# Kernel tuning notes

Measured on AMD Instinct MI355X. Metric: run time of the kernel, lower is better.

The kernel has to match this reference:

```python
import jax, jax.numpy as jnp
import numpy as np

B, NQ, NKV = 8, 2048, 2048
DQ, DKV, H = 1024, 1024, 256


def setup_inputs() -> dict:
    key = jax.random.key(0)
    ks = jax.random.split(key, 12)
    s = 0.02
    return {
        "x_q": jax.random.normal(ks[0], (B, NQ, DQ), jnp.float32),
        "x_kv": jax.random.normal(ks[1], (B, NKV, DKV), jnp.float32),
        "bias": jax.random.normal(ks[2], (B, NQ, NKV), jnp.float32),
        "wq_w": jax.random.normal(ks[3], (DQ, H), jnp.float32) * s,
        "wq_b": jnp.zeros((H,), jnp.float32),
        "wk_w": jax.random.normal(ks[4], (DKV, H), jnp.float32) * s,
        "wk_b": jnp.zeros((H,), jnp.float32),
        "wv_w": jax.random.normal(ks[5], (DKV, H), jnp.float32) * s,
        "wv_b": jnp.zeros((H,), jnp.float32),
        "f2_w": jax.random.normal(ks[6], (H, H), jnp.float32) * s,
        "f2_b": jnp.zeros((H,), jnp.float32),
    }


def reference(x_q, x_kv, bias, wq_w, wq_b, wk_w, wk_b, wv_w, wv_b, f2_w, f2_b):
    # Projections: [B, nq, H], [B, nkv, H]
    Q = jnp.einsum('bsd,dh->bsh', x_q, wq_w) + wq_b
    K = jnp.einsum('btd,dh->bth', x_kv, wk_w) + wk_b
    V = jnp.einsum('btd,dh->bth', x_kv, wv_w) + wv_b
    exp_w = jnp.exp(bias)          # [B, nq, nkv]
    exp_K = jnp.exp(K)             # [B, nkv, H]
    num = jnp.einsum('bst,bth->bsh', exp_w, exp_K * V)
    den = jnp.einsum('bst,bth->bsh', exp_w, exp_K)
    Yt = jax.nn.sigmoid(Q) * (num / den)
    return jnp.einsum('bsh,hg->bsg', Yt, f2_w) + f2_b
```

## Files before the change

kernel.cpp:

```cpp
#include <hip/hip_runtime.h>
#include <cstddef>
#include <cstdint>

#define BATCH 8
#define NQ    2048
#define NKV   2048
#define DIN   1024
#define HD    256

typedef __attribute__((ext_vector_type(8))) short bf16x8;
typedef __attribute__((ext_vector_type(4))) float f32x4;

__device__ __forceinline__ float sigmoidf_(float x) {
    return 1.0f / (1.0f + expf(-x));
}

__device__ __forceinline__ unsigned short f2bf(float f) {
    union { float f; unsigned int u; } v;
    v.f = f;
    unsigned int u = v.u;
    return (unsigned short)((u + 0x7FFFu + ((u >> 16) & 1u)) >> 16);
}

#define GLL16(gp, lp)                                                        \
    __builtin_amdgcn_global_load_lds(                                        \
        (const __attribute__((address_space(1))) void*)(gp),                 \
        (__attribute__((address_space(3))) void*)(lp), 16, 0, 0)

__device__ __forceinline__ f32x4 gload4(const float* p) {
    f32x4 r;
    asm volatile("global_load_dwordx4 %0, %1, off"
                 : "=v"(r) : "v"(p) : "memory");
    return r;
}

__global__ __launch_bounds__(256)
void wtrans_kernel(const float* __restrict__ w0, const float* __restrict__ w1,
                   const float* __restrict__ w2,
                   unsigned short* __restrict__ t0, unsigned short* __restrict__ t1,
                   unsigned short* __restrict__ t2)
{
    const float* w = (blockIdx.z == 0) ? w0 : (blockIdx.z == 1) ? w1 : w2;
    unsigned short* t = (blockIdx.z == 0) ? t0 : (blockIdx.z == 1) ? t1 : t2;
    const int k0 = blockIdx.y * 64;
    const int n0 = blockIdx.x * 64;
    const int tid = threadIdx.x;
    const int kq = tid >> 4;
    const int nq = tid & 15;
    float4 r[4];
#pragma unroll
    for (int i = 0; i < 4; ++i)
        r[i] = *(const float4*)&w[(size_t)(k0 + kq * 4 + i) * HD + n0 + nq * 4];
#pragma unroll
    for (int j = 0; j < 4; ++j) {
        ushort4 o;
        o.x = f2bf(((const float*)&r[0])[j]);
        o.y = f2bf(((const float*)&r[1])[j]);
        o.z = f2bf(((const float*)&r[2])[j]);
        o.w = f2bf(((const float*)&r[3])[j]);
        *(ushort4*)&t[(size_t)(n0 + nq * 4 + j) * DIN + k0 + kq * 4] = o;
    }
}

#define TS 64
#define TH 256
#define TK 32
#define A_LD 40

__global__ __launch_bounds__(256, 1)
void proj_q_mfma(const float* __restrict__ X,
                 const unsigned short* __restrict__ WT,
                 const float* __restrict__ bv,
                 float* __restrict__ sigQ)
{
    __shared__ unsigned short As[2][TS][A_LD];
    __shared__ unsigned short Bs[2][TH * TK];

    const int m0 = blockIdx.x * TS;
    const int tid = threadIdx.x;
    const int lane = tid & 63, wave = tid >> 6;
    const int quad = lane >> 4, l16 = lane & 15;

    const int a_row = tid >> 2, a_koff = (tid & 3) * 8;
    const float* aP = X + (size_t)(m0 + a_row) * DIN + a_koff;

    const unsigned short* bP[4];
    int ldsOff[4];
#pragma unroll
    for (int j = 0; j < 4; ++j) {
        int idx = j * 256 + tid;
        int row = idx >> 2, c = idx & 3;
        int kc = c ^ ((row >> 1) & 3);
        bP[j] = WT + (size_t)row * DIN + kc * 8;
        ldsOff[j] = (j * 256 + wave * 64) * 16;
    }

    f32x4 acc[4][4] = {};

#pragma unroll
    for (int j = 0; j < 4; ++j)
        GLL16(bP[j], (char*)&Bs[0][0] + ldsOff[j]);
    f32x4 c0 = gload4(aP);
    f32x4 c1 = gload4(aP + 4);
    f32x4 n0 = gload4(aP + TK);
    f32x4 n1 = gload4(aP + TK + 4);

    for (int k0 = 0; k0 < DIN; k0 += TK) {
        const int p = (k0 >> 5) & 1, pn = p ^ 1;
        const int kb = (k0 + TK < DIN) ? (k0 + TK) : (DIN - TK);
        const int km = (k0 + 2 * TK < DIN) ? (k0 + 2 * TK) : (DIN - TK);
        char* bL = (char*)&Bs[pn][0];
#pragma unroll
        for (int j = 0; j < 4; ++j)
            GLL16(bP[j] + kb, bL + ldsOff[j]);
        asm volatile("s_waitcnt vmcnt(4)" : "+v"(c0), "+v"(c1) :: "memory");
        ushort4 q0, q1;
        q0.x = f2bf(c0[0]); q0.y = f2bf(c0[1]); q0.z = f2bf(c0[2]); q0.w = f2bf(c0[3]);
        q1.x = f2bf(c1[0]); q1.y = f2bf(c1[1]); q1.z = f2bf(c1[2]); q1.w = f2bf(c1[3]);
        *(ushort4*)&As[p][a_row][a_koff]     = q0;
        *(ushort4*)&As[p][a_row][a_koff + 4] = q1;
        f32x4 m0v = gload4(aP + km);
        f32x4 m1v = gload4(aP + km + 4);
        asm volatile("s_waitcnt lgkmcnt(0)\ns_barrier" ::: "memory");
        bf16x8 af[4], bf[4];
#pragma unroll
        for (int rt = 0; rt < 4; ++rt)
            af[rt] = *(const bf16x8*)&As[p][rt * 16 + l16][quad * 8];
#pragma unroll
        for (int ct = 0; ct < 4; ++ct) {
            int row = wave * 64 + ct * 16 + l16;
            int off = row * 64 + ((quad ^ ((row >> 1) & 3)) * 16);
            bf[ct] = *(const bf16x8*)((const char*)&Bs[p][0] + off);
        }
#pragma unroll
        for (int rt = 0; rt < 4; ++rt)
#pragma unroll
            for (int ct = 0; ct < 4; ++ct)
                acc[rt][ct] = __builtin_amdgcn_mfma_f32_16x16x32_bf16(
                    af[rt], bf[ct], acc[rt][ct], 0, 0, 0);
        asm volatile("s_barrier" ::: "memory");
        c0 = n0; c1 = n1; n0 = m0v; n1 = m1v;
    }

#pragma unroll
    for (int rt = 0; rt < 4; ++rt)
#pragma unroll
        for (int ct = 0; ct < 4; ++ct) {
            const int h = wave * 64 + ct * 16 + l16;
            const float bb = bv[h];
#pragma unroll
            for (int r = 0; r < 4; ++r) {
                const int m = m0 + rt * 16 + quad * 4 + r;
                sigQ[(size_t)m * HD + h] = sigmoidf_(acc[rt][ct][r] + bb);
            }
        }
}

__global__ __launch_bounds__(256, 1)
void proj_kv_mfma(const float* __restrict__ X,
                  const unsigned short* __restrict__ WKT,
                  const float* __restrict__ bk,
                  const unsigned short* __restrict__ WVT,
                  const float* __restrict__ bvv,
                  unsigned short* __restrict__ eKt,
                  unsigned short* __restrict__ eKVt)
{
    __shared__ unsigned short As[2][TS][A_LD];
    __shared__ unsigned short Bk[2][TH * TK];
    __shared__ unsigned short Bv[2][TH * TK];

    const int m0 = blockIdx.x * TS;
    const int tid = threadIdx.x;
    const int lane = tid & 63, wave = tid >> 6;
    const int quad = lane >> 4, l16 = lane & 15;

    const int a_row = tid >> 2, a_koff = (tid & 3) * 8;
    const float* aP = X + (size_t)(m0 + a_row) * DIN + a_koff;

    const unsigned short* bkP[4];
    const unsigned short* bvP[4];
    int ldsOff[4];
#pragma unroll
    for (int j = 0; j < 4; ++j) {
        int idx = j * 256 + tid;
        int row = idx >> 2, c = idx & 3;
        int kc = c ^ ((row >> 1) & 3);
        bkP[j] = WKT + (size_t)row * DIN + kc * 8;
        bvP[j] = WVT + (size_t)row * DIN + kc * 8;
        ldsOff[j] = (j * 256 + wave * 64) * 16;
    }

    f32x4 acck[4][4] = {};
    f32x4 accv[4][4] = {};

#pragma unroll
    for (int j = 0; j < 4; ++j) {
        GLL16(bkP[j], (char*)&Bk[0][0] + ldsOff[j]);
        GLL16(bvP[j], (char*)&Bv[0][0] + ldsOff[j]);
    }
    f32x4 c0 = gload4(aP);
    f32x4 c1 = gload4(aP + 4);
    f32x4 n0 = gload4(aP + TK);
    f32x4 n1 = gload4(aP + TK + 4);

    for (int k0 = 0; k0 < DIN; k0 += TK) {
        const int p = (k0 >> 5) & 1, pn = p ^ 1;
        const int kb = (k0 + TK < DIN) ? (k0 + TK) : (DIN - TK);
        const int km = (k0 + 2 * TK < DIN) ? (k0 + 2 * TK) : (DIN - TK);
        char* bkL = (char*)&Bk[pn][0];
        char* bvL = (char*)&Bv[pn][0];
#pragma unroll
        for (int j = 0; j < 4; ++j) {
            GLL16(bkP[j] + kb, bkL + ldsOff[j]);
            GLL16(bvP[j] + kb, bvL + ldsOff[j]);
        }
        asm volatile("s_waitcnt vmcnt(8)" : "+v"(c0), "+v"(c1) :: "memory");
        ushort4 q0, q1;
        q0.x = f2bf(c0[0]); q0.y = f2bf(c0[1]); q0.z = f2bf(c0[2]); q0.w = f2bf(c0[3]);
        q1.x = f2bf(c1[0]); q1.y = f2bf(c1[1]); q1.z = f2bf(c1[2]); q1.w = f2bf(c1[3]);
        *(ushort4*)&As[p][a_row][a_koff]     = q0;
        *(ushort4*)&As[p][a_row][a_koff + 4] = q1;
        f32x4 m0v = gload4(aP + km);
        f32x4 m1v = gload4(aP + km + 4);
        asm volatile("s_waitcnt lgkmcnt(0)\ns_barrier" ::: "memory");
        bf16x8 af[4], bkf[4], bvf[4];
#pragma unroll
        for (int rt = 0; rt < 4; ++rt)
            af[rt] = *(const bf16x8*)&As[p][rt * 16 + l16][quad * 8];
#pragma unroll
        for (int ct = 0; ct < 4; ++ct) {
            int row = wave * 64 + ct * 16 + l16;
            int off = row * 64 + ((quad ^ ((row >> 1) & 3)) * 16);
            bkf[ct] = *(const bf16x8*)((const char*)&Bk[p][0] + off);
            bvf[ct] = *(const bf16x8*)((const char*)&Bv[p][0] + off);
        }
#pragma unroll
        for (int rt = 0; rt < 4; ++rt)
#pragma unroll
            for (int ct = 0; ct < 4; ++ct) {
                acck[rt][ct] = __builtin_amdgcn_mfma_f32_16x16x32_bf16(
                    af[rt], bkf[ct], acck[rt][ct], 0, 0, 0);
                accv[rt][ct] = __builtin_amdgcn_mfma_f32_16x16x32_bf16(
                    af[rt], bvf[ct], accv[rt][ct], 0, 0, 0);
            }
        asm volatile("s_barrier" ::: "memory");
        c0 = n0; c1 = n1; n0 = m0v; n1 = m1v;
    }

    const int bidx = m0 >> 11;
    const int tb = m0 & (NKV - 1);
#pragma unroll
    for (int rt = 0; rt < 4; ++rt)
#pragma unroll
        for (int ct = 0; ct < 4; ++ct) {
            const int h = wave * 64 + ct * 16 + l16;
            const float bkb = bk[h];
            const float bvb = bvv[h];
            ushort4 pk, pv;
            unsigned short* pK = (unsigned short*)&pk;
            unsigned short* pV = (unsigned short*)&pv;
#pragma unroll
            for (int r = 0; r < 4; ++r) {
                float e  = __expf(acck[rt][ct][r] + bkb);
                float ev = e * (accv[rt][ct][r] + bvb);
                pK[r] = f2bf(e);
                pV[r] = f2bf(ev);
            }
            const int t0 = tb + rt * 16 + quad * 4;
            size_t base = ((size_t)bidx * HD + h) * NKV + t0;
            *(ushort4*)&eKt[base]  = pk;
            *(ushort4*)&eKVt[base] = pv;
        }
}

__global__ __launch_bounds__(256, 1)
void aft_mfma_kernel(const float* __restrict__ bias,
                     const unsigned short* __restrict__ eKt,
                     const unsigned short* __restrict__ eKVt,
                     const float* __restrict__ sigQ,
                     float* __restrict__ Yt)
{
    __shared__ unsigned short As[2][TS][A_LD];
    __shared__ unsigned short Bn[2][TH * TK];
    __shared__ unsigned short Bd[2][TH * TK];

    const int lin = blockIdx.y * gridDim.x + blockIdx.x;
    const int b   = lin & 7;
    const int s0  = (lin >> 3) * TS;
    const int tid = threadIdx.x;
    const int lane = tid & 63, wave = tid >> 6;
    const int quad = lane >> 4, l16 = lane & 15;

    const int a_row = tid >> 2, a_koff = (tid & 3) * 8;
    const float* aP = bias + ((size_t)b * NQ + (s0 + a_row)) * NKV + a_koff;

    const unsigned short* bnP[4];
    const unsigned short* bdP[4];
    int ldsOff[4];
#pragma unroll
    for (int j = 0; j < 4; ++j) {
        int idx = j * 256 + tid;
        int row = idx >> 2, c = idx & 3;
        int kc = c ^ ((row >> 1) & 3);
        bnP[j] = eKVt + ((size_t)b * HD + row) * NKV + kc * 8;
        bdP[j] = eKt  + ((size_t)b * HD + row) * NKV + kc * 8;
        ldsOff[j] = (j * 256 + wave * 64) * 16;
    }

    f32x4 accn[4][4] = {};
    f32x4 accd[4][4] = {};

#pragma unroll
    for (int j = 0; j < 4; ++j) {
        GLL16(bnP[j], (char*)&Bn[0][0] + ldsOff[j]);
        GLL16(bdP[j], (char*)&Bd[0][0] + ldsOff[j]);
    }
    f32x4 c0 = gload4(aP);
    f32x4 c1 = gload4(aP + 4);
    f32x4 n0 = gload4(aP + TK);
    f32x4 n1 = gload4(aP + TK + 4);

    for (int k0 = 0; k0 < NKV; k0 += TK) {
        const int p = (k0 >> 5) & 1, pn = p ^ 1;
        const int kb = (k0 + TK < NKV) ? (k0 + TK) : (NKV - TK);
        const int km = (k0 + 2 * TK < NKV) ? (k0 + 2 * TK) : (NKV - TK);
        char* bnL = (char*)&Bn[pn][0];
        char* bdL = (char*)&Bd[pn][0];
#pragma unroll
        for (int j = 0; j < 4; ++j) {
            GLL16(bnP[j] + kb, bnL + ldsOff[j]);
            GLL16(bdP[j] + kb, bdL + ldsOff[j]);
        }
        asm volatile("s_waitcnt vmcnt(8)" : "+v"(c0), "+v"(c1) :: "memory");
        ushort4 q0, q1;
        q0.x = f2bf(__expf(c0[0])); q0.y = f2bf(__expf(c0[1]));
        q0.z = f2bf(__expf(c0[2])); q0.w = f2bf(__expf(c0[3]));
        q1.x = f2bf(__expf(c1[0])); q1.y = f2bf(__expf(c1[1]));
        q1.z = f2bf(__expf(c1[2])); q1.w = f2bf(__expf(c1[3]));
        *(ushort4*)&As[p][a_row][a_koff]     = q0;
        *(ushort4*)&As[p][a_row][a_koff + 4] = q1;
        f32x4 m0v = gload4(aP + km);
        f32x4 m1v = gload4(aP + km + 4);
        asm volatile("s_waitcnt lgkmcnt(0)\ns_barrier" ::: "memory");
        bf16x8 af[4], bnf[4], bdf[4];
#pragma unroll
        for (int rt = 0; rt < 4; ++rt)
            af[rt] = *(const bf16x8*)&As[p][rt * 16 + l16][quad * 8];
#pragma unroll
        for (int ct = 0; ct < 4; ++ct) {
            int row = wave * 64 + ct * 16 + l16;
            int off = row * 64 + ((quad ^ ((row >> 1) & 3)) * 16);
            bnf[ct] = *(const bf16x8*)((const char*)&Bn[p][0] + off);
            bdf[ct] = *(const bf16x8*)((const char*)&Bd[p][0] + off);
        }
#pragma unroll
        for (int rt = 0; rt < 4; ++rt)
#pragma unroll
            for (int ct = 0; ct < 4; ++ct) {
                accn[rt][ct] = __builtin_amdgcn_mfma_f32_16x16x32_bf16(
                    af[rt], bnf[ct], accn[rt][ct], 0, 0, 0);
                accd[rt][ct] = __builtin_amdgcn_mfma_f32_16x16x32_bf16(
                    af[rt], bdf[ct], accd[rt][ct], 0, 0, 0);
            }
        asm volatile("s_barrier" ::: "memory");
        c0 = n0; c1 = n1; n0 = m0v; n1 = m1v;
    }

#pragma unroll
    for (int rt = 0; rt < 4; ++rt)
#pragma unroll
        for (int ct = 0; ct < 4; ++ct) {
            const int h = wave * 64 + ct * 16 + l16;
#pragma unroll
            for (int r = 0; r < 4; ++r) {
                const int s = s0 + rt * 16 + quad * 4 + r;
                const size_t idx = ((size_t)b * NQ + s) * HD + h;
                Yt[idx] = sigQ[idx] * accn[rt][ct][r] / accd[rt][ct][r];
            }
        }
}

#define BM 64
#define BN 64
#define BK 16
#define PADF 4
#define LDAF (BM + PADF)
#define LDBF (BN + PADF)

__global__ __launch_bounds__(256)
void gemm_bias_kernel(const float* __restrict__ X, const float* __restrict__ W,
                      const float* __restrict__ bv, float* __restrict__ out,
                      int M, int N, int K)
{
    __shared__ float As[BK][LDAF];
    __shared__ float Ws[BK][LDBF];
    const int tid = threadIdx.x;
    const int tx = tid & 15, ty = tid >> 4;
    const int row0 = blockIdx.y * BM;
    const int col0 = blockIdx.x * BN;
    const int la_row = tid >> 2, la_col = (tid & 3) * 4;
    const int lw_row = tid >> 4, lw_col = (tid & 15) * 4;

    float acc[4][4] = {};

    const float* Xp = X + (size_t)(row0 + la_row) * K + la_col;
    const float* Wp = W + (size_t)lw_row * N + col0 + lw_col;

    float4 av = *(const float4*)Xp;
    float4 wv = *(const float4*)Wp;

    for (int k0 = 0; k0 < K; k0 += BK) {
        As[la_col + 0][la_row] = av.x;
        As[la_col + 1][la_row] = av.y;
        As[la_col + 2][la_row] = av.z;
        As[la_col + 3][la_row] = av.w;
        *(float4*)&Ws[lw_row][lw_col] = wv;
        __syncthreads();
        if (k0 + BK < K) {
            av = *(const float4*)(Xp + k0 + BK);
            wv = *(const float4*)(Wp + (size_t)(k0 + BK) * N);
        }
#pragma unroll
        for (int kk = 0; kk < BK; ++kk) {
            float4 a4 = *(const float4*)&As[kk][ty * 4];
            float4 w4 = *(const float4*)&Ws[kk][tx * 4];
            float aa[4] = {a4.x, a4.y, a4.z, a4.w};
            float ww[4] = {w4.x, w4.y, w4.z, w4.w};
#pragma unroll
            for (int i = 0; i < 4; ++i)
#pragma unroll
                for (int j = 0; j < 4; ++j)
                    acc[i][j] = fmaf(aa[i], ww[j], acc[i][j]);
        }
        __syncthreads();
    }

    float bb[4];
#pragma unroll
    for (int j = 0; j < 4; ++j) bb[j] = bv[col0 + tx * 4 + j];
#pragma unroll
    for (int i = 0; i < 4; ++i) {
        int r = row0 + ty * 4 + i;
        float4 o;
        o.x = acc[i][0] + bb[0];
        o.y = acc[i][1] + bb[1];
        o.z = acc[i][2] + bb[2];
        o.w = acc[i][3] + bb[3];
        *(float4*)&out[(size_t)r * N + col0 + tx * 4] = o;
    }
}

extern "C" void kernel_launch(void* const* d_in, const int* in_sizes, int n_in,
                              void* d_out, int out_size, void* d_ws, size_t ws_size,
                              hipStream_t stream)
{
    const float* x_q  = (const float*)d_in[0];
    const float* x_kv = (const float*)d_in[1];
    const float* bias = (const float*)d_in[2];
    const float* wq_w = (const float*)d_in[3];
    const float* wq_b = (const float*)d_in[4];
    const float* wk_w = (const float*)d_in[5];
    const float* wk_b = (const float*)d_in[6];
    const float* wv_w = (const float*)d_in[7];
    const float* wv_b = (const float*)d_in[8];
    const float* f2_w = (const float*)d_in[9];
    const float* f2_b = (const float*)d_in[10];
    float* out = (float*)d_out;

    float* ws = (float*)d_ws;
    const size_t nBH = (size_t)BATCH * NQ * HD;
    float* sigQ = ws;
    float* Yt   = ws + nBH;
    unsigned short* eKt  = (unsigned short*)(ws + 2 * nBH);
    unsigned short* eKVt = eKt + nBH;
    unsigned short* wqT  = eKVt + nBH;
    unsigned short* wkT  = wqT + (size_t)HD * DIN;
    unsigned short* wvT  = wkT + (size_t)HD * DIN;

    const int M = BATCH * NQ;
    dim3 blk(256);

    wtrans_kernel<<<dim3(HD / 64, DIN / 64, 3), blk, 0, stream>>>(
        wq_w, wk_w, wv_w, wqT, wkT, wvT);

    proj_q_mfma<<<dim3(M / TS), blk, 0, stream>>>(x_q, wqT, wq_b, sigQ);

    proj_kv_mfma<<<dim3(M / TS), blk, 0, stream>>>(
        x_kv, wkT, wk_b, wvT, wv_b, eKt, eKVt);

    aft_mfma_kernel<<<dim3(NQ / TS, BATCH), blk, 0, stream>>>(
        bias, eKt, eKVt, sigQ, Yt);

    gemm_bias_kernel<<<dim3(HD / BN, M / BM), blk, 0, stream>>>(
        Yt, f2_w, f2_b, out, M, HD, HD);
}
```

Baseline: 456.7 us.

## Pre-tile and pre-swizzle B operands in global memory for contiguous LDS loads

Weight transposes and the exp(K)/exp(K)*V intermediates are now written in a K-tile-major layout (32-wide k tiles of 256 rows, with the XOR swizzle already applied). Each GEMM's global-to-LDS B-tile load then reads one contiguous 16 KB block per tile instead of 64-byte pieces spread across rows with a large stride. This is meant to improve DRAM/L2 access efficiency for the B-operand streams. In exchange, the producer kernels' stores become more scattered, and the layout assumptions are coupled across all kernels.

After: 445.0 us. 1.03x faster.

```diff
diff --git a/kernel.cpp b/kernel.cpp
--- a/kernel.cpp
+++ b/kernel.cpp
@@ -33,6 +33,7 @@
                  : "=v"(r) : "v"(p) : "memory");
     return r;
 }
+
 
 __global__ __launch_bounds__(256)
 void wtrans_kernel(const float* __restrict__ w0, const float* __restrict__ w1,
@@ -51,14 +52,19 @@
 #pragma unroll
     for (int i = 0; i < 4; ++i)
         r[i] = *(const float4*)&w[(size_t)(k0 + kq * 4 + i) * HD + n0 + nq * 4];
-#pragma unroll
-    for (int j = 0; j < 4; ++j) {
+    const int k = k0 + kq * 4;
+    const int kt = k >> 5;
+    const int c  = (k & 31) >> 3;
+#pragma unroll
+    for (int j = 0; j < 4; ++j) {
+        const int h = n0 + nq * 4 + j;
         ushort4 o;
         o.x = f2bf(((const float*)&r[0])[j]);
         o.y = f2bf(((const float*)&r[1])[j]);
         o.z = f2bf(((const float*)&r[2])[j]);
         o.w = f2bf(((const float*)&r[3])[j]);
-        *(ushort4*)&t[(size_t)(n0 + nq * 4 + j) * DIN + k0 + kq * 4] = o;
+        const int kc = c ^ ((h >> 1) & 3);
+        *(ushort4*)&t[((size_t)kt * 256 + h) * 32 + kc * 8 + (k & 7)] = o;
     }
 }
 
@@ -88,10 +94,7 @@
     int ldsOff[4];
 #pragma unroll
     for (int j = 0; j < 4; ++j) {
-        int idx = j * 256 + tid;
-        int row = idx >> 2, c = idx & 3;
-        int kc = c ^ ((row >> 1) & 3);
-        bP[j] = WT + (size_t)row * DIN + kc * 8;
+        bP[j] = WT + ((size_t)j * 256 + tid) * 8;
         ldsOff[j] = (j * 256 + wave * 64) * 16;
     }
 
@@ -112,7 +115,7 @@
         char* bL = (char*)&Bs[pn][0];
 #pragma unroll
         for (int j = 0; j < 4; ++j)
-            GLL16(bP[j] + kb, bL + ldsOff[j]);
+            GLL16(bP[j] + (size_t)kb * 256, bL + ldsOff[j]);
         asm volatile("s_waitcnt vmcnt(4)" : "+v"(c0), "+v"(c1) :: "memory");
         ushort4 q0, q1;
         q0.x = f2bf(c0[0]); q0.y = f2bf(c0[1]); q0.z = f2bf(c0[2]); q0.w = f2bf(c0[3]);
@@ -182,11 +185,8 @@
     int ldsOff[4];
 #pragma unroll
     for (int j = 0; j < 4; ++j) {
-        int idx = j * 256 + tid;
-        int row = idx >> 2, c = idx & 3;
-        int kc = c ^ ((row >> 1) & 3);
-        bkP[j] = WKT + (size_t)row * DIN + kc * 8;
-        bvP[j] = WVT + (size_t)row * DIN + kc * 8;
+        bkP[j] = WKT + ((size_t)j * 256 + tid) * 8;
+        bvP[j] = WVT + ((size_t)j * 256 + tid) * 8;
         ldsOff[j] = (j * 256 + wave * 64) * 16;
     }
 
@@ -211,8 +211,8 @@
         char* bvL = (char*)&Bv[pn][0];
 #pragma unroll
         for (int j = 0; j < 4; ++j) {
-            GLL16(bkP[j] + kb, bkL + ldsOff[j]);
-            GLL16(bvP[j] + kb, bvL + ldsOff[j]);
+            GLL16(bkP[j] + (size_t)kb * 256, bkL + ldsOff[j]);
+            GLL16(bvP[j] + (size_t)kb * 256, bvL + ldsOff[j]);
         }
         asm volatile("s_waitcnt vmcnt(8)" : "+v"(c0), "+v"(c1) :: "memory");
         ushort4 q0, q1;
@@ -266,10 +266,13 @@
                 pK[r] = f2bf(e);
                 pV[r] = f2bf(ev);
             }
-            const int t0 = tb + rt * 16 + quad * 4;
-            size_t base = ((size_t)bidx * HD + h) * NKV + t0;
-            *(ushort4*)&eKt[base]  = pk;
-            *(ushort4*)&eKVt[base] = pv;
+            const int t0a = tb + rt * 16 + quad * 4;
+            const int tt = t0a >> 5, tc = t0a & 31;
+            const int kc = (tc >> 3) ^ ((h >> 1) & 3);
+            size_t idx = (((size_t)bidx * (NKV / 32) + tt) * 256 + h) * 32
+                         + kc * 8 + (tc & 7);
+            *(ushort4*)&eKt[idx]  = pk;
+            *(ushort4*)&eKVt[idx] = pv;
         }
 }
 
@@ -299,11 +302,9 @@
     int ldsOff[4];
 #pragma unroll
     for (int j = 0; j < 4; ++j) {
-        int idx = j * 256 + tid;
-        int row = idx >> 2, c = idx & 3;
-        int kc = c ^ ((row >> 1) & 3);
-        bnP[j] = eKVt + ((size_t)b * HD + row) * NKV + kc * 8;
-        bdP[j] = eKt  + ((size_t)b * HD + row) * NKV + kc * 8;
+        const size_t base = (size_t)b * (NKV / 32) * 256 * 32;
+        bnP[j] = eKVt + base + ((size_t)j * 256 + tid) * 8;
+        bdP[j] = eKt  + base + ((size_t)j * 256 + tid) * 8;
         ldsOff[j] = (j * 256 + wave * 64) * 16;
     }
 
@@ -328,8 +329,8 @@
         char* bdL = (char*)&Bd[pn][0];
 #pragma unroll
         for (int j = 0; j < 4; ++j) {
-            GLL16(bnP[j] + kb, bnL + ldsOff[j]);
-            GLL16(bdP[j] + kb, bdL + ldsOff[j]);
+            GLL16(bnP[j] + (size_t)kb * 256, bnL + ldsOff[j]);
+            GLL16(bdP[j] + (size_t)kb * 256, bdL + ldsOff[j]);
         }
         asm volatile("s_waitcnt vmcnt(8)" : "+v"(c0), "+v"(c1) :: "memory");
         ushort4 q0, q1;
```
